# Kernel optimization log

Hardware: AMD Instinct MI355X
Metric: run time of the kernel (lower is better)

## Reference

```python
import jax, jax.numpy as jnp
import numpy as np

EPS = 1e-5
GROUPS = 16


def _deform_conv_gn(input, offset, mask, weight, bias, gamma, beta):
    # Modulated deformable conv v2 (k=3, stride=1, pad=1) + GroupNorm(16).
    B, C, H, W = input.shape
    Co = weight.shape[0]
    K = 9
    # kernel taps relative to center (pad=1 cancels the -1 origin shift)
    ky = jnp.repeat(jnp.arange(3) - 1, 3).astype(input.dtype)   # [9]
    kx = jnp.tile(jnp.arange(3) - 1, 3).astype(input.dtype)     # [9]
    off = offset.reshape(B, K, 2, H, W)                          # (dy, dx) per tap
    dy, dx = off[:, :, 0], off[:, :, 1]                          # [B,9,H,W]
    y = jnp.arange(H, dtype=input.dtype)[None, None, :, None] + ky[None, :, None, None] + dy
    x = jnp.arange(W, dtype=input.dtype)[None, None, None, :] + kx[None, :, None, None] + dx
    y0 = jnp.floor(y)
    x0 = jnp.floor(x)
    flat = input.reshape(B, C, H * W)

    def corner(yc, xc):
        # zero-padded bilinear corner gather -> [B,C,9,H,W]
        valid = ((yc >= 0) & (yc < H) & (xc >= 0) & (xc < W)).astype(input.dtype)
        yi = jnp.clip(yc, 0, H - 1).astype(jnp.int32)
        xi = jnp.clip(xc, 0, W - 1).astype(jnp.int32)
        idx = (yi * W + xi).reshape(B, -1)
        g = jax.vmap(lambda im, ix: jnp.take(im, ix, axis=1))(flat, idx)
        return g.reshape(B, C, K, H, W) * valid[:, None]

    wy1 = y - y0
    wx1 = x - x0
    wy0 = 1.0 - wy1
    wx0 = 1.0 - wx1
    val = (corner(y0, x0) * (wy0 * wx0)[:, None]
           + corner(y0, x0 + 1.0) * (wy0 * wx1)[:, None]
           + corner(y0 + 1.0, x0) * (wy1 * wx0)[:, None]
           + corner(y0 + 1.0, x0 + 1.0) * (wy1 * wx1)[:, None])
    cols = val * mask[:, None]                                   # modulation [B,C,9,H,W]
    out = jnp.einsum('bckhw,ock->bohw', cols, weight.reshape(Co, C, K))
    out = out + bias[None, :, None, None]
    # GroupNorm(16)
    g = out.reshape(B, GROUPS, Co // GROUPS, H, W)
    mu = g.mean(axis=(2, 3, 4), keepdims=True)
    var = g.var(axis=(2, 3, 4), keepdims=True)
    g = (g - mu) * jax.lax.rsqrt(var + EPS)
    return g.reshape(B, Co, H, W) * gamma[None, :, None, None] + beta[None, :, None, None]


def setup_inputs() -> dict:
    key = jax.random.key(0)
    k1, k2, k3, k4 = jax.random.split(key, 4)
    B, C, Co, H, W = 4, 256, 256, 64, 64
    return {
        'input': jax.random.normal(k1, (B, C, H, W), dtype=jnp.float32),
        'offset': jax.random.normal(k2, (B, 18, H, W), dtype=jnp.float32),
        'mask': jax.random.uniform(k3, (B, 9, H, W), dtype=jnp.float32),
        'weight': jax.random.normal(k4, (Co, C, 3, 3), dtype=jnp.float32) * 0.02,
        'bias': jnp.zeros((Co,), dtype=jnp.float32),
        'gamma': jnp.ones((Co,), dtype=jnp.float32),
        'beta': jnp.zeros((Co,), dtype=jnp.float32),
    }


def reference(input, offset, mask, weight, bias, gamma, beta):
    return _deform_conv_gn(input, offset, mask, weight, bias, gamma, beta)
```

## Files before the change

kernel.cpp:

```cpp
#include <hip/hip_runtime.h>

typedef __attribute__((ext_vector_type(8))) short short8;
typedef __attribute__((ext_vector_type(4))) float f32x4;

#define Bsz 4
#define Cin 256
#define Cout 256
#define Hh 64
#define Ww 64
#define HW 4096
#define NG 16
#define EPSV 1e-5f

#define CSTR 40

static __device__ __forceinline__ unsigned f2bf(float f) {
    unsigned u = __float_as_uint(f);
    return (u + 0x7fffu + ((u >> 16) & 1u)) >> 16;
}

static __device__ __forceinline__ float2 ld8(const float* p) {
    float2 v;
    __builtin_memcpy(&v, p, 8);
    return v;
}

__global__ void wt_kernel(const float* __restrict__ w, ushort* __restrict__ wtb,
                          float* __restrict__ stats) {
    const int i = blockIdx.x * 256 + threadIdx.x;
    if (blockIdx.x == 0 && threadIdx.x < 128) stats[threadIdx.x] = 0.f;
    if (i >= Cout * Cin * 9) return;
    const int o = i / (Cin * 9);
    const int rem = i % (Cin * 9);
    const int c = rem / 9, kk = rem % 9;
    const int ks = kk * 8 + (c >> 5);
    wtb[(ks * 256 + o) * 32 + (c & 31)] = (ushort)f2bf(w[i]);
}

__launch_bounds__(512, 2)
__global__ void dcn_kernel(const float* __restrict__ in,
                           const float* __restrict__ offs,
                           const float* __restrict__ mask,
                           const ushort* __restrict__ wtb,
                           const float* __restrict__ bias,
                           float* __restrict__ out,
                           float* __restrict__ stats) {
    __shared__ int2   s_ta[9 * 64];
    __shared__ float4 s_tw[9 * 64];
    __shared__ ushort s_col[2][64 * CSTR];

    const int t  = threadIdx.x;
    const int bx = blockIdx.x;
    const int q  = bx & 7, r = bx >> 3;
    const int b  = q >> 1;
    const int h  = ((q & 1) << 5) | r;
    const int lane = t & 63;
    const int wv   = t >> 6;
    const int n    = lane;
    const int quad = lane >> 4;
    const int l15  = lane & 15;

    for (int j = t; j < 576; j += 512) {
        const int k = j >> 6, p = j & 63;
        const float* ob = offs + (size_t)b * 18 * HW + h * Ww + p;
        const float dy = ob[(2 * k) * HW];
        const float dx = ob[(2 * k + 1) * HW];
        const float m  = mask[((size_t)b * 9 + k) * HW + h * Ww + p];
        const float y = (float)h + (float)(k / 3 - 1) + dy;
        const float x = (float)p + (float)(k % 3 - 1) + dx;
        const float y0f = floorf(y), x0f = floorf(x);
        const float ly = y - y0f, lx = x - x0f;
        const float hy = 1.f - ly, hx = 1.f - lx;
        const int y0 = (int)y0f, x0 = (int)x0f;
        const int yc0 = min(max(y0, 0), 63);
        const int yc1 = min(max(y0 + 1, 0), 63);
        const int xb  = min(max(x0, 0), 62);
        float ax = 0.f, ay = 0.f;
        if (x0 == xb) {
            ax = hx;
            ay = lx;
        } else if (x0 < xb) {
            ax = (x0 + 1 == 0) ? lx : 0.f;
        } else {
            ay = (x0 == 63) ? hx : 0.f;
        }
        const float w0 = (y0 >= 0 && y0 < 64) ? m * hy : 0.f;
        const float w1 = (y0 + 1 >= 0 && y0 + 1 < 64) ? m * ly : 0.f;
        s_ta[j] = make_int2(yc0 * 64 + xb, yc1 * 64 + xb);
        s_tw[j] = make_float4(w0 * ax, w0 * ay, w1 * ax, w1 * ay);
    }
    __syncthreads();

    f32x4 acc[2][4];
#pragma unroll
    for (int i = 0; i < 2; i++)
#pragma unroll
        for (int nt = 0; nt < 4; nt++) acc[i][nt] = (f32x4){0.f, 0.f, 0.f, 0.f};

    const float* inb = in + (size_t)b * Cin * HW;

#define GATHER(cc, kk, pk0, pk1)                                           \
    {                                                                      \
        const int2  ad = s_ta[(kk) * 64 + n];                              \
        const float4 tw = s_tw[(kk) * 64 + n];                             \
        const float* cb = inb + (size_t)((cc) * 32 + wv * 4) * HW;         \
        float vv[4];                                                       \
        _Pragma("unroll")                                                  \
        for (int j = 0; j < 4; j++) {                                      \
            const float* pl = cb + j * HW;                                 \
            const float2 g0 = ld8(pl + ad.x);                              \
            const float2 g1 = ld8(pl + ad.y);                              \
            vv[j] = tw.x * g0.x + tw.y * g0.y + tw.z * g1.x + tw.w * g1.y; \
        }                                                                  \
        pk0 = f2bf(vv[0]) | (f2bf(vv[1]) << 16);                           \
        pk1 = f2bf(vv[2]) | (f2bf(vv[3]) << 16);                           \
    }

    unsigned pk0, pk1;
    GATHER(0, 0, pk0, pk1);

    int p = 0;
#pragma unroll 1
    for (int s = 0; s < 72; s++) {
        const int cc = s / 9;
        const int kk = s - cc * 9;
        const int ks = kk * 8 + cc;
        *(unsigned long long*)&s_col[p][n * CSTR + wv * 4] =
            (unsigned long long)pk0 | ((unsigned long long)pk1 << 32);
        __syncthreads();
        if (s < 71) {
            const int s1 = s + 1;
            const int cc1 = s1 / 9;
            GATHER(cc1, s1 - cc1 * 9, pk0, pk1);
        }
        const ushort* wp = wtb + ((size_t)(ks * 256 + wv * 32 + l15)) * 32 + quad * 8;
        const short8 a0 = *(const short8*)wp;
        const short8 a1 = *(const short8*)(wp + 16 * 32);
        short8 bfr[4];
#pragma unroll
        for (int nt = 0; nt < 4; nt++)
            bfr[nt] = *(const short8*)&s_col[p][(nt * 16 + l15) * CSTR + quad * 8];
#pragma unroll
        for (int nt = 0; nt < 4; nt++) {
            acc[0][nt] = __builtin_amdgcn_mfma_f32_16x16x32_bf16(a0, bfr[nt], acc[0][nt], 0, 0, 0);
            acc[1][nt] = __builtin_amdgcn_mfma_f32_16x16x32_bf16(a1, bfr[nt], acc[1][nt], 0, 0, 0);
        }
        p ^= 1;
    }
#undef GATHER

    float gs[2], gq[2];
#pragma unroll
    for (int i = 0; i < 2; i++) {
        float s = 0.f, qq = 0.f;
        const int ob = wv * 32 + i * 16 + quad * 4;
#pragma unroll
        for (int reg = 0; reg < 4; reg++) {
            const int o = ob + reg;
            const float bv = bias[o];
            float* op = out + ((size_t)(b * 256 + o)) * HW + h * Ww + l15;
#pragma unroll
            for (int nt = 0; nt < 4; nt++) {
                const float v = acc[i][nt][reg] + bv;
                op[nt * 16] = v;
                s += v;
                qq += v * v;
            }
        }
        gs[i] = s; gq[i] = qq;
    }
#pragma unroll
    for (int off = 32; off; off >>= 1) {
        gs[0] += __shfl_xor(gs[0], off);
        gq[0] += __shfl_xor(gq[0], off);
        gs[1] += __shfl_xor(gs[1], off);
        gq[1] += __shfl_xor(gq[1], off);
    }
    if (lane == 0) {
#pragma unroll
        for (int i = 0; i < 2; i++) {
            const int g = wv * 2 + i;
            atomicAdd(&stats[((size_t)b * NG + g) * 2],     gs[i]);
            atomicAdd(&stats[((size_t)b * NG + g) * 2 + 1], gq[i]);
        }
    }
}

__global__ void gn_apply_kernel(float* __restrict__ x, const float* __restrict__ stats,
                                const float* __restrict__ gamma,
                                const float* __restrict__ beta) {
    const int i = blockIdx.x * 256 + threadIdx.x;
    const int plane = i >> 10;
    const int o = plane & 255;
    const int bg = plane >> 4;
    const float s = stats[bg * 2], q = stats[bg * 2 + 1];
    const float inv_n = 1.f / 65536.f;
    const float mu = s * inv_n;
    const float var = q * inv_n - mu * mu;
    const float rs = rsqrtf(var + EPSV);
    const float ga = gamma[o] * rs;
    const float be = beta[o] - mu * ga;
    float4 v = ((float4*)x)[i];
    v.x = v.x * ga + be;
    v.y = v.y * ga + be;
    v.z = v.z * ga + be;
    v.w = v.w * ga + be;
    ((float4*)x)[i] = v;
}

extern "C" void kernel_launch(void* const* d_in, const int* in_sizes, int n_in,
                              void* d_out, int out_size, void* d_ws, size_t ws_size,
                              hipStream_t stream) {
    const float* input  = (const float*)d_in[0];
    const float* offset = (const float*)d_in[1];
    const float* maskp  = (const float*)d_in[2];
    const float* weight = (const float*)d_in[3];
    const float* bias   = (const float*)d_in[4];
    const float* gamma  = (const float*)d_in[5];
    const float* beta   = (const float*)d_in[6];
    float* out = (float*)d_out;

    ushort* wtb  = (ushort*)d_ws;
    float* stats = (float*)((char*)d_ws + (size_t)Cout * Cin * 9 * sizeof(ushort));

    hipLaunchKernelGGL(wt_kernel, dim3((Cout * Cin * 9 + 255) / 256), dim3(256), 0,
                       stream, weight, wtb, stats);
    hipLaunchKernelGGL(dcn_kernel, dim3(Bsz * Hh), dim3(512), 0, stream,
                       input, offset, maskp, wtb, bias, out, stats);
    hipLaunchKernelGGL(gn_apply_kernel, dim3((Bsz * Cout * HW / 4) / 256), dim3(256), 0,
                       stream, out, stats, gamma, beta);
}
```

Measured before the change: 216.8 us.

## Split DCN tiles into quarter-row blocks with 256 threads and deferred gather combine

```diff
diff --git a/kernel.cpp b/kernel.cpp
--- a/kernel.cpp
+++ b/kernel.cpp
@@ -12,6 +12,7 @@
 #define NG 16
 #define EPSV 1e-5f
 
+#define QP 16
 #define CSTR 40
 
 static __device__ __forceinline__ unsigned f2bf(float f) {
@@ -37,7 +38,7 @@
     wtb[(ks * 256 + o) * 32 + (c & 31)] = (ushort)f2bf(w[i]);
 }
 
-__launch_bounds__(512, 2)
+__launch_bounds__(256, 4)
 __global__ void dcn_kernel(const float* __restrict__ in,
                            const float* __restrict__ offs,
                            const float* __restrict__ mask,
@@ -45,29 +46,30 @@
                            const float* __restrict__ bias,
                            float* __restrict__ out,
                            float* __restrict__ stats) {
-    __shared__ int2   s_ta[9 * 64];
-    __shared__ float4 s_tw[9 * 64];
-    __shared__ ushort s_col[2][64 * CSTR];
+    __shared__ int2   s_ta[9 * QP];
+    __shared__ float4 s_tw[9 * QP];
+    __shared__ ushort s_col[2][2 * QP * CSTR];
 
     const int t  = threadIdx.x;
     const int bx = blockIdx.x;
     const int q  = bx & 7, r = bx >> 3;
     const int b  = q >> 1;
-    const int h  = ((q & 1) << 5) | r;
+    const int h  = ((q & 1) << 5) | (r >> 2);
+    const int n0 = (r & 3) * QP;
     const int lane = t & 63;
     const int wv   = t >> 6;
-    const int n    = lane;
     const int quad = lane >> 4;
     const int l15  = lane & 15;
 
-    for (int j = t; j < 576; j += 512) {
-        const int k = j >> 6, p = j & 63;
-        const float* ob = offs + (size_t)b * 18 * HW + h * Ww + p;
+    if (t < 9 * QP) {
+        const int k = t / QP, p = t % QP;
+        const int wq = n0 + p;
+        const float* ob = offs + (size_t)b * 18 * HW + h * Ww + wq;
         const float dy = ob[(2 * k) * HW];
         const float dx = ob[(2 * k + 1) * HW];
-        const float m  = mask[((size_t)b * 9 + k) * HW + h * Ww + p];
+        const float m  = mask[((size_t)b * 9 + k) * HW + h * Ww + wq];
         const float y = (float)h + (float)(k / 3 - 1) + dy;
-        const float x = (float)p + (float)(k % 3 - 1) + dx;
+        const float x = (float)wq + (float)(k % 3 - 1) + dx;
         const float y0f = floorf(y), x0f = floorf(x);
         const float ly = y - y0f, lx = x - x0f;
         const float hy = 1.f - ly, hx = 1.f - lx;
@@ -77,8 +79,7 @@
         const int xb  = min(max(x0, 0), 62);
         float ax = 0.f, ay = 0.f;
         if (x0 == xb) {
-            ax = hx;
-            ay = lx;
+            ax = hx; ay = lx;
         } else if (x0 < xb) {
             ax = (x0 + 1 == 0) ? lx : 0.f;
         } else {
@@ -86,102 +87,108 @@
         }
         const float w0 = (y0 >= 0 && y0 < 64) ? m * hy : 0.f;
         const float w1 = (y0 + 1 >= 0 && y0 + 1 < 64) ? m * ly : 0.f;
-        s_ta[j] = make_int2(yc0 * 64 + xb, yc1 * 64 + xb);
-        s_tw[j] = make_float4(w0 * ax, w0 * ay, w1 * ax, w1 * ay);
+        s_ta[t] = make_int2(yc0 * 64 + xb, yc1 * 64 + xb);
+        s_tw[t] = make_float4(w0 * ax, w0 * ay, w1 * ax, w1 * ay);
     }
     __syncthreads();
 
-    f32x4 acc[2][4];
-#pragma unroll
-    for (int i = 0; i < 2; i++)
-#pragma unroll
-        for (int nt = 0; nt < 4; nt++) acc[i][nt] = (f32x4){0.f, 0.f, 0.f, 0.f};
+    const int gn_ = t & 15;
+    const int cg  = t >> 4;
+    const int kh_w = cg >> 3, c8 = cg & 7;
+    ushort* wslot = &s_col[0][kh_w * (QP * CSTR) + gn_ * CSTR + c8 * 4];
+    const int wslot_stride = 2 * QP * CSTR;
+
+    f32x4 acc[4];
+#pragma unroll
+    for (int mt = 0; mt < 4; mt++) acc[mt] = (f32x4){0.f, 0.f, 0.f, 0.f};
 
     const float* inb = in + (size_t)b * Cin * HW;
 
-#define GATHER(cc, kk, pk0, pk1)                                           \
+#define GISSUE(ccq, kk, g)                                                 \
     {                                                                      \
-        const int2  ad = s_ta[(kk) * 64 + n];                              \
-        const float4 tw = s_tw[(kk) * 64 + n];                             \
-        const float* cb = inb + (size_t)((cc) * 32 + wv * 4) * HW;         \
-        float vv[4];                                                       \
+        const int2 ad = s_ta[(kk) * QP + gn_];                             \
+        const float* cb = inb + (size_t)((ccq) * 64 + cg * 4) * HW;        \
         _Pragma("unroll")                                                  \
         for (int j = 0; j < 4; j++) {                                      \
             const float* pl = cb + j * HW;                                 \
-            const float2 g0 = ld8(pl + ad.x);                              \
-            const float2 g1 = ld8(pl + ad.y);                              \
-            vv[j] = tw.x * g0.x + tw.y * g0.y + tw.z * g1.x + tw.w * g1.y; \
+            g[2 * j]     = ld8(pl + ad.x);                                 \
+            g[2 * j + 1] = ld8(pl + ad.y);                                 \
         }                                                                  \
-        pk0 = f2bf(vv[0]) | (f2bf(vv[1]) << 16);                           \
-        pk1 = f2bf(vv[2]) | (f2bf(vv[3]) << 16);                           \
-    }
-
-    unsigned pk0, pk1;
-    GATHER(0, 0, pk0, pk1);
-
-    int p = 0;
+    }
+
+    float2 g[8];
+    GISSUE(0, 0, g);
+
+    int pbuf = 0;
 #pragma unroll 1
-    for (int s = 0; s < 72; s++) {
-        const int cc = s / 9;
-        const int kk = s - cc * 9;
-        const int ks = kk * 8 + cc;
-        *(unsigned long long*)&s_col[p][n * CSTR + wv * 4] =
-            (unsigned long long)pk0 | ((unsigned long long)pk1 << 32);
+    for (int s = 0; s < 36; s++) {
+        const int ccq = s / 9;
+        const int kk  = s - ccq * 9;
+        const int ks0 = kk * 8 + ccq * 2;
+
+        short8 afr[4][2];
+        {
+            const ushort* wp0 = wtb + ((size_t)(ks0 * 256 + wv * 64 + l15)) * 32 + quad * 8;
+#pragma unroll
+            for (int mt = 0; mt < 4; mt++)
+#pragma unroll
+                for (int kh = 0; kh < 2; kh++)
+                    afr[mt][kh] = *(const short8*)(wp0 + (kh * 256 + mt * 16) * 32);
+        }
+
+        {
+            const float4 tw = s_tw[kk * QP + gn_];
+            float vv[4];
+#pragma unroll
+            for (int j = 0; j < 4; j++)
+                vv[j] = tw.x * g[2 * j].x + tw.y * g[2 * j].y +
+                        tw.z * g[2 * j + 1].x + tw.w * g[2 * j + 1].y;
+            const unsigned pk0 = f2bf(vv[0]) | (f2bf(vv[1]) << 16);
+            const unsigned pk1 = f2bf(vv[2]) | (f2bf(vv[3]) << 16);
+            *(unsigned long long*)(wslot + pbuf * wslot_stride) =
+                (unsigned long long)pk0 | ((unsigned long long)pk1 << 32);
+        }
         __syncthreads();
-        if (s < 71) {
+
+        if (s < 35) {
             const int s1 = s + 1;
-            const int cc1 = s1 / 9;
-            GATHER(cc1, s1 - cc1 * 9, pk0, pk1);
-        }
-        const ushort* wp = wtb + ((size_t)(ks * 256 + wv * 32 + l15)) * 32 + quad * 8;
-        const short8 a0 = *(const short8*)wp;
-        const short8 a1 = *(const short8*)(wp + 16 * 32);
-        short8 bfr[4];
-#pragma unroll
-        for (int nt = 0; nt < 4; nt++)
-            bfr[nt] = *(const short8*)&s_col[p][(nt * 16 + l15) * CSTR + quad * 8];
-#pragma unroll
-        for (int nt = 0; nt < 4; nt++) {
-            acc[0][nt] = __builtin_amdgcn_mfma_f32_16x16x32_bf16(a0, bfr[nt], acc[0][nt], 0, 0, 0);
-            acc[1][nt] = __builtin_amdgcn_mfma_f32_16x16x32_bf16(a1, bfr[nt], acc[1][nt], 0, 0, 0);
-        }
-        p ^= 1;
-    }
-#undef GATHER
-
-    float gs[2], gq[2];
-#pragma unroll
-    for (int i = 0; i < 2; i++) {
-        float s = 0.f, qq = 0.f;
-        const int ob = wv * 32 + i * 16 + quad * 4;
+            const int ccq1 = s1 / 9;
+            GISSUE(ccq1, s1 - ccq1 * 9, g);
+        }
+
+        short8 bfr[2];
+#pragma unroll
+        for (int kh = 0; kh < 2; kh++)
+            bfr[kh] = *(const short8*)&s_col[pbuf][kh * (QP * CSTR) + l15 * CSTR + quad * 8];
+#pragma unroll
+        for (int mt = 0; mt < 4; mt++) {
+            acc[mt] = __builtin_amdgcn_mfma_f32_16x16x32_bf16(afr[mt][0], bfr[0], acc[mt], 0, 0, 0);
+            acc[mt] = __builtin_amdgcn_mfma_f32_16x16x32_bf16(afr[mt][1], bfr[1], acc[mt], 0, 0, 0);
+        }
+        pbuf ^= 1;
+    }
+#undef GISSUE
+
+#pragma unroll
+    for (int mt = 0; mt < 4; mt++) {
+        float sg = 0.f, qg = 0.f;
 #pragma unroll
         for (int reg = 0; reg < 4; reg++) {
-            const int o = ob + reg;
-            const float bv = bias[o];
-            float* op = out + ((size_t)(b * 256 + o)) * HW + h * Ww + l15;
-#pragma unroll
-            for (int nt = 0; nt < 4; nt++) {
-                const float v = acc[i][nt][reg] + bv;
-                op[nt * 16] = v;
-                s += v;
-                qq += v * v;
-            }
-        }
-        gs[i] = s; gq[i] = qq;
-    }
-#pragma unroll
-    for (int off = 32; off; off >>= 1) {
-        gs[0] += __shfl_xor(gs[0], off);
-        gq[0] += __shfl_xor(gq[0], off);
-        gs[1] += __shfl_xor(gs[1], off);
-        gq[1] += __shfl_xor(gq[1], off);
-    }
-    if (lane == 0) {
-#pragma unroll
-        for (int i = 0; i < 2; i++) {
-            const int g = wv * 2 + i;
-            atomicAdd(&stats[((size_t)b * NG + g) * 2],     gs[i]);
-            atomicAdd(&stats[((size_t)b * NG + g) * 2 + 1], gq[i]);
+            const int o = wv * 64 + mt * 16 + quad * 4 + reg;
+            const float v = acc[mt][reg] + bias[o];
+            out[((size_t)(b * 256 + o)) * HW + h * Ww + n0 + l15] = v;
+            sg += v;
+            qg += v * v;
+        }
+#pragma unroll
+        for (int off = 32; off; off >>= 1) {
+            sg += __shfl_xor(sg, off);
+            qg += __shfl_xor(qg, off);
+        }
+        if (lane == 0) {
+            const int grp = wv * 4 + mt;
+            atomicAdd(&stats[((size_t)b * NG + grp) * 2],     sg);
+            atomicAdd(&stats[((size_t)b * NG + grp) * 2 + 1], qg);
         }
     }
 }
@@ -193,10 +200,10 @@
     const int plane = i >> 10;
     const int o = plane & 255;
     const int bg = plane >> 4;
-    const float s = stats[bg * 2], q = stats[bg * 2 + 1];
+    const float s = stats[bg * 2], qv = stats[bg * 2 + 1];
     const float inv_n = 1.f / 65536.f;
     const float mu = s * inv_n;
-    const float var = q * inv_n - mu * mu;
+    const float var = qv * inv_n - mu * mu;
     const float rs = rsqrtf(var + EPSV);
     const float ga = gamma[o] * rs;
     const float be = beta[o] - mu * ga;
@@ -225,7 +232,7 @@
 
     hipLaunchKernelGGL(wt_kernel, dim3((Cout * Cin * 9 + 255) / 256), dim3(256), 0,
                        stream, weight, wtb, stats);
-    hipLaunchKernelGGL(dcn_kernel, dim3(Bsz * Hh), dim3(512), 0, stream,
+    hipLaunchKernelGGL(dcn_kernel, dim3(Bsz * Hh * 4), dim3(256), 0, stream,
                        input, offset, maskp, wtb, bias, out, stats);
     hipLaunchKernelGGL(gn_apply_kernel, dim3((Bsz * Cout * HW / 4) / 256), dim3(256), 0,
                        stream, out, stats, gamma, beta);
```

Result: slower. 271.4 us (+25.2%).

## Stage a 16-row input window per channel chunk in LDS for bilinear gathers

Applied to the files above, without the earlier changes.

```diff
diff --git a/kernel.cpp b/kernel.cpp
--- a/kernel.cpp
+++ b/kernel.cpp
@@ -13,16 +13,12 @@
 #define EPSV 1e-5f
 
 #define CSTR 40
+#define WROWS 16
+#define PCH 32
 
 static __device__ __forceinline__ unsigned f2bf(float f) {
     unsigned u = __float_as_uint(f);
     return (u + 0x7fffu + ((u >> 16) & 1u)) >> 16;
-}
-
-static __device__ __forceinline__ float2 ld8(const float* p) {
-    float2 v;
-    __builtin_memcpy(&v, p, 8);
-    return v;
 }
 
 __global__ void wt_kernel(const float* __restrict__ w, ushort* __restrict__ wtb,
@@ -45,9 +41,10 @@
                            const float* __restrict__ bias,
                            float* __restrict__ out,
                            float* __restrict__ stats) {
+    __shared__ float  s_in[PCH * WROWS * 64];
+    __shared__ ushort s_col[2][64 * CSTR];
     __shared__ int2   s_ta[9 * 64];
     __shared__ float4 s_tw[9 * 64];
-    __shared__ ushort s_col[2][64 * CSTR];
 
     const int t  = threadIdx.x;
     const int bx = blockIdx.x;
@@ -56,9 +53,21 @@
     const int h  = ((q & 1) << 5) | r;
     const int lane = t & 63;
     const int wv   = t >> 6;
-    const int n    = lane;
     const int quad = lane >> 4;
     const int l15  = lane & 15;
+    const int gn   = lane;
+    const int cg   = wv;
+
+    const float* inb = in + (size_t)b * Cin * HW;
+
+    float4 st[16];
+#pragma unroll
+    for (int i = 0; i < 16; i++) {
+        const int idx = i * 512 + t;
+        const int p = idx >> 8, sl = (idx >> 4) & 15, qq = idx & 15;
+        const int row = min(max(h - 8 + sl, 0), 63);
+        st[i] = *(const float4*)(inb + (size_t)p * HW + row * 64 + qq * 4);
+    }
 
     for (int j = t; j < 576; j += 512) {
         const int k = j >> 6, p = j & 63;
@@ -77,8 +86,7 @@
         const int xb  = min(max(x0, 0), 62);
         float ax = 0.f, ay = 0.f;
         if (x0 == xb) {
-            ax = hx;
-            ay = lx;
+            ax = hx; ay = lx;
         } else if (x0 < xb) {
             ax = (x0 + 1 == 0) ? lx : 0.f;
         } else {
@@ -86,68 +94,109 @@
         }
         const float w0 = (y0 >= 0 && y0 < 64) ? m * hy : 0.f;
         const float w1 = (y0 + 1 >= 0 && y0 + 1 < 64) ? m * ly : 0.f;
-        s_ta[j] = make_int2(yc0 * 64 + xb, yc1 * 64 + xb);
+        const int s0 = yc0 - (h - 8), s1 = yc1 - (h - 8);
+        int2 ta;
+        if (s0 >= 0 && s0 < WROWS && s1 >= 0 && s1 < WROWS)
+            ta = make_int2(s0 * 64 + xb, s1 * 64 + xb);
+        else
+            ta = make_int2(-1 - (yc0 * 64 + xb), yc1 * 64 + xb);
+        s_ta[j] = ta;
         s_tw[j] = make_float4(w0 * ax, w0 * ay, w1 * ax, w1 * ay);
     }
+
+#pragma unroll
+    for (int i = 0; i < 16; i++) {
+        const int idx = i * 512 + t;
+        const int p = idx >> 8, sl = (idx >> 4) & 15, qq = idx & 15;
+        *(float4*)&s_in[p * 1024 + sl * 64 + qq * 4] = st[i];
+    }
     __syncthreads();
 
+    int2   rta[9];
+    float4 rtw[9];
+#pragma unroll
+    for (int k = 0; k < 9; k++) {
+        rta[k] = s_ta[k * 64 + gn];
+        rtw[k] = s_tw[k * 64 + gn];
+    }
+
     f32x4 acc[2][4];
 #pragma unroll
     for (int i = 0; i < 2; i++)
 #pragma unroll
         for (int nt = 0; nt < 4; nt++) acc[i][nt] = (f32x4){0.f, 0.f, 0.f, 0.f};
 
-    const float* inb = in + (size_t)b * Cin * HW;
-
-#define GATHER(cc, kk, pk0, pk1)                                           \
-    {                                                                      \
-        const int2  ad = s_ta[(kk) * 64 + n];                              \
-        const float4 tw = s_tw[(kk) * 64 + n];                             \
-        const float* cb = inb + (size_t)((cc) * 32 + wv * 4) * HW;         \
-        float vv[4];                                                       \
-        _Pragma("unroll")                                                  \
-        for (int j = 0; j < 4; j++) {                                      \
-            const float* pl = cb + j * HW;                                 \
-            const float2 g0 = ld8(pl + ad.x);                              \
-            const float2 g1 = ld8(pl + ad.y);                              \
-            vv[j] = tw.x * g0.x + tw.y * g0.y + tw.z * g1.x + tw.w * g1.y; \
-        }                                                                  \
-        pk0 = f2bf(vv[0]) | (f2bf(vv[1]) << 16);                           \
-        pk1 = f2bf(vv[2]) | (f2bf(vv[3]) << 16);                           \
-    }
-
-    unsigned pk0, pk1;
-    GATHER(0, 0, pk0, pk1);
-
-    int p = 0;
+    const int colw_off = gn * CSTR + ((((cg >> 1) ^ (gn >> 4)) & 3) << 3) + ((cg & 1) << 2);
+
+    int pbuf = 0;
 #pragma unroll 1
-    for (int s = 0; s < 72; s++) {
-        const int cc = s / 9;
-        const int kk = s - cc * 9;
-        const int ks = kk * 8 + cc;
-        *(unsigned long long*)&s_col[p][n * CSTR + wv * 4] =
-            (unsigned long long)pk0 | ((unsigned long long)pk1 << 32);
-        __syncthreads();
-        if (s < 71) {
-            const int s1 = s + 1;
-            const int cc1 = s1 / 9;
-            GATHER(cc1, s1 - cc1 * 9, pk0, pk1);
-        }
-        const ushort* wp = wtb + ((size_t)(ks * 256 + wv * 32 + l15)) * 32 + quad * 8;
-        const short8 a0 = *(const short8*)wp;
-        const short8 a1 = *(const short8*)(wp + 16 * 32);
-        short8 bfr[4];
-#pragma unroll
-        for (int nt = 0; nt < 4; nt++)
-            bfr[nt] = *(const short8*)&s_col[p][(nt * 16 + l15) * CSTR + quad * 8];
-#pragma unroll
-        for (int nt = 0; nt < 4; nt++) {
-            acc[0][nt] = __builtin_amdgcn_mfma_f32_16x16x32_bf16(a0, bfr[nt], acc[0][nt], 0, 0, 0);
-            acc[1][nt] = __builtin_amdgcn_mfma_f32_16x16x32_bf16(a1, bfr[nt], acc[1][nt], 0, 0, 0);
-        }
-        p ^= 1;
-    }
-#undef GATHER
+    for (int c = 0; c < 8; c++) {
+#pragma unroll 1
+        for (int kk = 0; kk < 9; kk++) {
+            const int ks = kk * 8 + c;
+            const ushort* wp = wtb + ((size_t)(ks * 256 + wv * 32 + l15)) * 32 + quad * 8;
+            const short8 a0 = *(const short8*)wp;
+            const short8 a1 = *(const short8*)(wp + 16 * 32);
+
+            float vv[4];
+            const int2   ad = rta[kk];
+            const float4 tw = rtw[kk];
+            if (ad.x >= 0) {
+#pragma unroll
+                for (int j = 0; j < 4; j++) {
+                    const float* pb = &s_in[(cg * 4 + j) * (WROWS * 64)];
+                    vv[j] = tw.x * pb[ad.x] + tw.y * pb[ad.x + 1] +
+                            tw.z * pb[ad.y] + tw.w * pb[ad.y + 1];
+                }
+            } else {
+                const int gx0 = -1 - ad.x;
+#pragma unroll
+                for (int j = 0; j < 4; j++) {
+                    const float* pb = inb + (size_t)(c * 32 + cg * 4 + j) * HW;
+                    vv[j] = tw.x * pb[gx0] + tw.y * pb[gx0 + 1] +
+                            tw.z * pb[ad.y] + tw.w * pb[ad.y + 1];
+                }
+            }
+
+            if (kk == 8 && c < 7) {
+#pragma unroll
+                for (int i = 0; i < 16; i++) {
+                    const int idx = i * 512 + t;
+                    const int p = idx >> 8, sl = (idx >> 4) & 15, qq = idx & 15;
+                    const int row = min(max(h - 8 + sl, 0), 63);
+                    st[i] = *(const float4*)(inb + (size_t)((c + 1) * 32 + p) * HW +
+                                             row * 64 + qq * 4);
+                }
+            }
+
+            const unsigned pk0 = f2bf(vv[0]) | (f2bf(vv[1]) << 16);
+            const unsigned pk1 = f2bf(vv[2]) | (f2bf(vv[3]) << 16);
+            *(unsigned long long*)&s_col[pbuf][colw_off] =
+                (unsigned long long)pk0 | ((unsigned long long)pk1 << 32);
+            __syncthreads();
+
+            short8 bfr[4];
+#pragma unroll
+            for (int nt = 0; nt < 4; nt++)
+                bfr[nt] = *(const short8*)&s_col[pbuf][(nt * 16 + l15) * CSTR +
+                                                       ((quad ^ nt) << 3)];
+#pragma unroll
+            for (int nt = 0; nt < 4; nt++) {
+                acc[0][nt] = __builtin_amdgcn_mfma_f32_16x16x32_bf16(a0, bfr[nt], acc[0][nt], 0, 0, 0);
+                acc[1][nt] = __builtin_amdgcn_mfma_f32_16x16x32_bf16(a1, bfr[nt], acc[1][nt], 0, 0, 0);
+            }
+            pbuf ^= 1;
+        }
+        if (c < 7) {
+#pragma unroll
+            for (int i = 0; i < 16; i++) {
+                const int idx = i * 512 + t;
+                const int p = idx >> 8, sl = (idx >> 4) & 15, qq = idx & 15;
+                *(float4*)&s_in[p * 1024 + sl * 64 + qq * 4] = st[i];
+            }
+            __syncthreads();
+        }
+    }
 
     float gs[2], gq[2];
 #pragma unroll
@@ -193,10 +242,10 @@
     const int plane = i >> 10;
     const int o = plane & 255;
     const int bg = plane >> 4;
-    const float s = stats[bg * 2], q = stats[bg * 2 + 1];
+    const float s = stats[bg * 2], qv = stats[bg * 2 + 1];
     const float inv_n = 1.f / 65536.f;
     const float mu = s * inv_n;
-    const float var = q * inv_n - mu * mu;
+    const float var = qv * inv_n - mu * mu;
     const float rs = rsqrtf(var + EPSV);
     const float ga = gamma[o] * rs;
     const float be = beta[o] - mu * ga;
```

Result: slower. 290.3 us (+33.9%).
